# Optimization experiments

Hardware: AMD Instinct MI355X
Metric: run time of the kernel (lower is better)

## Reference

```python
import jax, jax.numpy as jnp
import numpy as np

WH = 7; WW = 7; N = WH * WW          # window tokens
C = 256; H = 8; D = C // H            # dim, heads, head_dim
SCALE = D ** -0.5
B = 4096                              # batch * num_windows
EPS = 1e-12


def _relative_position_index():
    coords = np.stack(np.meshgrid(np.arange(WH), np.arange(WW), indexing='ij'))  # [2,WH,WW]
    cf = coords.reshape(2, -1)                                                   # [2,N]
    rc = (cf[:, :, None] - cf[:, None, :]).transpose(1, 2, 0).astype(np.int64)   # [N,N,2]
    rc[..., 0] += WH - 1
    rc[..., 1] += WW - 1
    rc[..., 0] *= 2 * WW - 1
    return jnp.asarray(rc.sum(-1), jnp.int32)                                    # [N,N]


def _l2n_heads(x):
    # F.normalize default dim=1: normalize over the HEADS axis of [B,H,N,D]
    n = jnp.sqrt(jnp.sum(x * x, axis=1, keepdims=True))
    return x / jnp.maximum(n, EPS)


def setup_inputs() -> dict:
    key = jax.random.key(0)
    ks = jax.random.split(key, 12)
    p = lambda k, s: (0.02 * jax.random.normal(k, s, dtype=jnp.float32))
    return {
        'x1': jax.random.normal(ks[0], (B, N, C), dtype=jnp.float32),
        'x2': jax.random.normal(ks[1], (B, N, C), dtype=jnp.float32),
        'rel_index': _relative_position_index(),
        'kv1_w': p(ks[2], (2 * C, C)), 'kv1_b': jnp.zeros((2 * C,), jnp.float32),
        'kv2_w': p(ks[3], (2 * C, C)), 'kv2_b': jnp.zeros((2 * C,), jnp.float32),
        'q_w': p(ks[4], (C, C)), 'q_b': jnp.zeros((C,), jnp.float32),
        'rpb_table': p(ks[5], ((2 * WH - 1) * (2 * WW - 1), H)),
        'proj1_w': p(ks[6], (C, C)), 'proj1_b': jnp.zeros((C,), jnp.float32),
        'proj2_w': p(ks[7], (C, C)), 'proj2_b': jnp.zeros((C,), jnp.float32),
    }


def reference(x1, x2, rel_index, kv1_w, kv1_b, kv2_w, kv2_b, q_w, q_b,
              rpb_table, proj1_w, proj1_b, proj1=None, proj2=None, **_unused):
    del proj1, proj2
    raise NotImplementedError


def _forward(x1, x2, rel_index, kv1_w, kv1_b, kv2_w, kv2_b, q_w, q_b,
             rpb_table, proj1_w, proj1_b, proj2_w, proj2_b):
    def split_kv(x, w, b):
        kv = (x @ w.T + b).reshape(B, N, 2, H, D).transpose(2, 0, 3, 1, 4)  # [2,B,H,N,D]
        return kv[0], kv[1]

    k1, v1 = split_kv(x1, kv1_w, kv1_b)
    k2, v2 = split_kv(x2, kv2_w, kv2_b)

    q = (jnp.abs(x2 - x1) @ q_w.T + q_b).reshape(B, N, H, D).transpose(0, 2, 1, 3)  # [B,H,N,D]
    q = q * SCALE

    bias = rpb_table[rel_index.reshape(-1)].reshape(N, N, H).transpose(2, 0, 1)  # [H,N,N]

    # branch 1: attend q -> k2/v2
    attn = jnp.einsum('bhnd,bhmd->bhnm', _l2n_heads(q), _l2n_heads(k2)) + bias[None]
    attn = jax.nn.softmax(attn, axis=-1)
    o1 = (jnp.einsum('bhnm,bhmd->bhnd', attn, v2) - q).transpose(0, 2, 1, 3).reshape(B, N, C)
    o1 = o1 @ proj1_w.T + proj1_b

    # branch 2: q rescaled again, attend -> k1/v1
    q = q * SCALE
    attn = jnp.einsum('bhnd,bhmd->bhnm', _l2n_heads(q), _l2n_heads(k1)) + bias[None]
    attn = jax.nn.softmax(attn, axis=-1)
    o2 = (jnp.einsum('bhnm,bhmd->bhnd', attn, v1) - q).transpose(0, 2, 1, 3).reshape(B, N, C)
    o2 = o2 @ proj2_w.T + proj2_b
    return o1, o2


def reference(x1, x2, rel_index, kv1_w, kv1_b, kv2_w, kv2_b, q_w, q_b,
              rpb_table, proj1_w, proj1_b, proj2_w, proj2_b):
    return _forward(x1, x2, rel_index, kv1_w, kv1_b, kv2_w, kv2_b, q_w, q_b,
                    rpb_table, proj1_w, proj1_b, proj2_w, proj2_b)
```

## Files before the change

kernel.cpp:

```cpp
#include <hip/hip_runtime.h>
#include <hip/hip_bf16.h>


typedef __attribute__((ext_vector_type(8))) short short8;
typedef __attribute__((ext_vector_type(4))) float f32x4;

#define NTOK 49
#define NWIN 4096
#define MROWS 200704
#define NMT 3136
#define SCALE 0.17677669529663687f

#define TQ_T   0
#define TKV1_T 16
#define TKV2_T 48
#define TP1_T  80
#define TP2_T  96

#define OFF_BIAS_B 917504ull
#define OFF_QN_B   1048576ull
#define OFF_NRM_B  103809024ull
#define OFF_KN2_B  129499136ull
#define OFF_KN1_B  232259584ull
#define OFF_V2_B   335020032ull
#define OFF_V1_B   437780480ull

__device__ __forceinline__ short f2b(float f) {
    union { float f; unsigned u; } v{f};
    unsigned r = v.u + 0x7fffu + ((v.u >> 16) & 1u);
    return (short)(r >> 16);
}
__device__ __forceinline__ float b2f(short s) {
    return __uint_as_float(((unsigned)(unsigned short)s) << 16);
}
__device__ __forceinline__ short8 pack8(float4 a, float4 b) {
    short8 s;
    s[0]=f2b(a.x); s[1]=f2b(a.y); s[2]=f2b(a.z); s[3]=f2b(a.w);
    s[4]=f2b(b.x); s[5]=f2b(b.y); s[6]=f2b(b.z); s[7]=f2b(b.w);
    return s;
}
__device__ __forceinline__ f32x4 mfma16(short8 a, short8 b, f32x4 c) {
    return __builtin_amdgcn_mfma_f32_16x16x32_bf16(a, b, c, 0, 0, 0);
}
__device__ __forceinline__ short8 g16(const short* p) { return *(const short8*)p; }
__device__ __forceinline__ short8 ld16r128(const short* base, int row, int m8) {
    return *(const short8*)((const char*)base + row*128 + ((m8*2) ^ ((row&7)<<4)));
}
__device__ __forceinline__ void st2r128(short* base, int row, int m, short v) {
    *(short*)((char*)base + row*128 + ((m*2) ^ ((row&7)<<4))) = v;
}
__device__ __forceinline__ void gl16(const void* g, void* l) {
    __builtin_amdgcn_global_load_lds(
        (const __attribute__((address_space(1))) unsigned*)g,
        (__attribute__((address_space(3))) unsigned*)l, 16, 0, 0);
}
__device__ __forceinline__ short8 ldb(const short* tile, int lr, int lg, int kb) {
    return *(const short8*)((const char*)tile + lr*512
                            + ((kb*64 + lg*16) ^ ((lr&7)<<4)));
}

__global__ void prep_w(const float* __restrict__ qw, const float* __restrict__ kv1,
                       const float* __restrict__ kv2, const float* __restrict__ p1,
                       const float* __restrict__ p2, short* __restrict__ ws) {
    int i = blockIdx.x * 256 + threadIdx.x;
    int e = i * 8;
    const float* src; int rel, tbase;
    if      (e < 65536)  { src = qw;  rel = e;          tbase = TQ_T;  }
    else if (e < 196608) { src = kv1; rel = e - 65536;  tbase = TKV1_T; }
    else if (e < 327680) { src = kv2; rel = e - 196608; tbase = TKV2_T; }
    else if (e < 393216) { src = p1;  rel = e - 327680; tbase = TP1_T; }
    else                 { src = p2;  rel = e - 393216; tbase = TP2_T; }
    int row = rel >> 8, col = rel & 255;
    short8 v;
#pragma unroll
    for (int k = 0; k < 8; ++k) v[k] = f2b(src[rel + k]);
    char* dst = (char*)ws + (size_t)(tbase + (row >> 4)) * 8192
              + (row & 15) * 512 + ((col * 2) ^ ((row & 7) << 4));
    *(short8*)dst = v;
}

__global__ void k_bias(const int* __restrict__ rel_index,
                       const float* __restrict__ rpb, short* __restrict__ ws) {
    int i = blockIdx.x * 256 + threadIdx.x;
    int r  = i & 3;
    int nt = (i >> 2) & 3;
    int lr = (i >> 4) & 15;
    int lg = (i >> 8) & 3;
    int mt = (i >> 10) & 3;
    int h  = (i >> 12) & 7;
    int m  = 16*mt + 4*lg + r;
    int mc = 16*nt + lr;
    float v = 0.f;
    if (m < NTOK && mc < NTOK) v = rpb[rel_index[m*NTOK + mc]*8 + h];
    ((float*)((char*)ws + OFF_BIAS_B))[i] = v;
}

__global__ __launch_bounds__(256, 3)
void k_qkv(const float* __restrict__ x1, const float* __restrict__ x2,
           const float* __restrict__ kv1_b, const float* __restrict__ kv2_b,
           const float* __restrict__ q_b, short* __restrict__ ws)
{
    __shared__ short Bt[2][4096];

    const int t    = (int)threadIdx.x;
    const int wv   = t >> 6;
    const int lane = t & 63;
    const int lr   = t & 15;
    const int lg   = (t >> 4) & 3;
    const int bid  = (int)blockIdx.x;
    const int type = bid % 3;
    const int mt   = bid / 3;
    const int ar   = mt*64 + 16*wv + lr;

    unsigned widr[4], tokr[4];
#pragma unroll
    for (int r = 0; r < 4; ++r) {
        unsigned n = (unsigned)(mt*64 + 16*wv + 4*lg + r);
        widr[r] = n / 49u; tokr[r] = n - widr[r]*49u;
    }

    const char* tb = (const char*)ws
        + (size_t)(type == 0 ? TQ_T : (type == 1 ? TKV2_T : TKV1_T)) * 8192;

#define STAGE(J, B) do {                                                  \
        const char* g_ = tb + (size_t)(J)*8192 + wv*2048 + lane*16;       \
        char* l_ = (char*)Bt[(B)] + wv*2048 + lane*16;                    \
        gl16(g_, l_); gl16(g_ + 1024, l_ + 1024);                         \
    } while (0)

    if (type == 0) {
        short8 ad[8];
#pragma unroll
        for (int kb = 0; kb < 8; ++kb) {
            const float* pa = x2 + (size_t)ar*256 + kb*32 + lg*8;
            const float* pc = x1 + (size_t)ar*256 + kb*32 + lg*8;
            float4 a0 = *(const float4*)pa, a1 = *(const float4*)(pa+4);
            float4 c0 = *(const float4*)pc, c1 = *(const float4*)(pc+4);
            float4 d0 = make_float4(fabsf(a0.x-c0.x), fabsf(a0.y-c0.y),
                                    fabsf(a0.z-c0.z), fabsf(a0.w-c0.w));
            float4 d1 = make_float4(fabsf(a1.x-c1.x), fabsf(a1.y-c1.y),
                                    fabsf(a1.z-c1.z), fabsf(a1.w-c1.w));
            ad[kb] = pack8(d0, d1);
        }
        STAGE(0, 0);
        __syncthreads();
        f32x4 qa[16];
#pragma unroll
        for (int j = 0; j < 16; ++j) {
            if (j < 15) STAGE(j+1, (j+1)&1);
            const short* bt = Bt[j&1];
            f32x4 acc = {0.f,0.f,0.f,0.f};
#pragma unroll
            for (int kb = 0; kb < 8; ++kb) acc = mfma16(ad[kb], ldb(bt, lr, lg, kb), acc);
            float bj = q_b[j*16 + lr];
#pragma unroll
            for (int r = 0; r < 4; ++r) acc[r] = (acc[r] + bj) * SCALE;
            qa[j] = acc;
            __syncthreads();
        }
        short* qn  = (short*)((char*)ws + OFF_QN_B);
        float* nrm = (float*)((char*)ws + OFF_NRM_B);
#pragma unroll
        for (int r = 0; r < 4; ++r) {
            float s0 = 0.f, s1 = 0.f;
#pragma unroll
            for (int jj = 0; jj < 8; ++jj) {
                float v0 = qa[2*jj][r], v1 = qa[2*jj+1][r];
                s0 = fmaf(v0, v0, s0); s1 = fmaf(v1, v1, s1);
            }
            float n0 = fmaxf(sqrtf(s0), 1e-12f), n1 = fmaxf(sqrtf(s1), 1e-12f);
            unsigned n = widr[r]*49u + tokr[r];
            nrm[(size_t)n*32 + lr]      = n0;
            nrm[(size_t)n*32 + 16 + lr] = n1;
            float ri0 = 1.0f/n0, ri1 = 1.0f/n1;
            size_t base = ((size_t)widr[r]*392 + tokr[r])*32;
#pragma unroll
            for (int j = 0; j < 16; ++j) {
                int h = j >> 1, p = j & 1;
                qn[base + h*1568 + 16*p + lr] = f2b(qa[j][r] * (p ? ri1 : ri0));
            }
        }
    } else {
        const float* xp  = (type == 1) ? x2 : x1;
        const float* kvb = (type == 1) ? kv2_b : kv1_b;
        short* knp = (short*)((char*)ws + ((type == 1) ? OFF_KN2_B : OFF_KN1_B));
        short* vp  = (short*)((char*)ws + ((type == 1) ? OFF_V2_B  : OFF_V1_B));

        short8 ad[8];
#pragma unroll
        for (int kb = 0; kb < 8; ++kb) {
            const float* pa = xp + (size_t)ar*256 + kb*32 + lg*8;
            float4 a0 = *(const float4*)pa, a1 = *(const float4*)(pa+4);
            ad[kb] = pack8(a0, a1);
        }
        size_t base[4];
#pragma unroll
        for (int r = 0; r < 4; ++r) base[r] = ((size_t)widr[r]*392 + tokr[r])*32;

        STAGE(0, 0);
        __syncthreads();
        f32x4 ka[16];
#pragma unroll
        for (int j = 0; j < 32; ++j) {
            if (j < 31) STAGE(j+1, (j+1)&1);
            const short* bt = Bt[j&1];
            f32x4 acc = {0.f,0.f,0.f,0.f};
#pragma unroll
            for (int kb = 0; kb < 8; ++kb) acc = mfma16(ad[kb], ldb(bt, lr, lg, kb), acc);
            if (j < 16) {
                float bj = kvb[j*16 + lr];
#pragma unroll
                for (int r = 0; r < 4; ++r) acc[r] += bj;
                ka[j] = acc;
            } else {
                const int jv = j - 16;
                float bj = kvb[256 + jv*16 + lr];
                int h = jv >> 1, p = jv & 1;
#pragma unroll
                for (int r = 0; r < 4; ++r)
                    vp[base[r] + h*1568 + 16*p + lr] = f2b(acc[r] + bj);
            }
            __syncthreads();
        }
#pragma unroll
        for (int r = 0; r < 4; ++r) {
            float s0 = 0.f, s1 = 0.f;
#pragma unroll
            for (int jj = 0; jj < 8; ++jj) {
                float v0 = ka[2*jj][r], v1 = ka[2*jj+1][r];
                s0 = fmaf(v0, v0, s0); s1 = fmaf(v1, v1, s1);
            }
            float ri0 = 1.0f/fmaxf(sqrtf(s0), 1e-12f);
            float ri1 = 1.0f/fmaxf(sqrtf(s1), 1e-12f);
#pragma unroll
            for (int j = 0; j < 16; ++j) {
                int h = j >> 1, p = j & 1;
                knp[base[r] + h*1568 + 16*p + lr] = f2b(ka[j][r] * (p ? ri1 : ri0));
            }
        }
    }
#undef STAGE
}

__global__ __launch_bounds__(512, 2)
void k_attn(short* __restrict__ ws)
{
    __shared__ short OP[NTOK*256];
    __shared__ short PS[8*16*64];

    const int t  = (int)threadIdx.x;
    const int h  = t >> 6;
    const int lr = t & 15;
    const int lg = (t >> 4) & 3;
    const int bid = (int)blockIdx.x;
    const int wid = bid >> 1;
    const int br  = bid & 1;

    const short* qn  = (const short*)((const char*)ws + OFF_QN_B);
    const float* nrm = (const float*)((const char*)ws + OFF_NRM_B);
    const float* bias_t = (const float*)((const char*)ws + OFF_BIAS_B);
    short* Pb = PS + h*1024;
    const int khbase = (wid*8 + h)*49;

    const short* knp = (const short*)((const char*)ws + (br ? OFF_KN1_B : OFF_KN2_B));
    const short* vp  = (const short*)((const char*)ws + (br ? OFF_V1_B  : OFF_V2_B));
    short* opre = (short*)((char*)ws + (br ? OFF_KN1_B : OFF_KN2_B));
    const float subscale = br ? SCALE : 1.0f;

    short8 kf[4];
#pragma unroll
    for (int nt = 0; nt < 4; ++nt) {
        int n = min(16*nt + lr, NTOK-1);
        kf[nt] = g16(knp + (size_t)(khbase + n)*32 + lg*8);
    }
    short8 vf[2][2];
#pragma unroll
    for (int dt = 0; dt < 2; ++dt)
#pragma unroll
        for (int st = 0; st < 2; ++st) {
            short8 s8;
#pragma unroll
            for (int e = 0; e < 8; ++e) {
                int tok = st*32 + lg*8 + e;
                short v_ = 0;
                if (tok < NTOK) v_ = vp[(size_t)(khbase + tok)*32 + 16*dt + lr];
                s8[e] = v_;
            }
            vf[dt][st] = s8;
        }

#pragma unroll 1
    for (int mt = 0; mt < 4; ++mt) {
        int mrow = min(16*mt + lr, NTOK-1);
        short8 aq = g16(qn + (size_t)(khbase + mrow)*32 + lg*8);
        f32x4 S[4];
#pragma unroll
        for (int nt = 0; nt < 4; ++nt) {
            f32x4 z = {0.f,0.f,0.f,0.f};
            S[nt] = mfma16(aq, kf[nt], z);
        }
        const float4* bp4 = (const float4*)(bias_t + ((((h*4 + mt)*4 + lg)*16) + lr)*16);
        float4 bv[4];
#pragma unroll
        for (int nt = 0; nt < 4; ++nt) bv[nt] = bp4[nt];
        float sv[4][4];
#pragma unroll
        for (int nt = 0; nt < 4; ++nt) {
            bool ms = (16*nt + lr) >= NTOK;
            sv[nt][0] = ms ? -1e30f : (S[nt][0] + bv[nt].x);
            sv[nt][1] = ms ? -1e30f : (S[nt][1] + bv[nt].y);
            sv[nt][2] = ms ? -1e30f : (S[nt][2] + bv[nt].z);
            sv[nt][3] = ms ? -1e30f : (S[nt][3] + bv[nt].w);
        }
        float isum[4];
#pragma unroll
        for (int r = 0; r < 4; ++r) {
            float mx = fmaxf(fmaxf(sv[0][r], sv[1][r]), fmaxf(sv[2][r], sv[3][r]));
#pragma unroll
            for (int d = 1; d < 16; d <<= 1) mx = fmaxf(mx, __shfl_xor(mx, d));
            float e0 = __expf(sv[0][r]-mx), e1 = __expf(sv[1][r]-mx);
            float e2 = __expf(sv[2][r]-mx), e3 = __expf(sv[3][r]-mx);
            float sm = (e0+e1) + (e2+e3);
#pragma unroll
            for (int d = 1; d < 16; d <<= 1) sm += __shfl_xor(sm, d);
            isum[r] = 1.0f / sm;
            int pr = 4*lg + r;
            st2r128(Pb, pr,      lr, f2b(e0));
            st2r128(Pb, pr, 16 + lr, f2b(e1));
            st2r128(Pb, pr, 32 + lr, f2b(e2));
            st2r128(Pb, pr, 48 + lr, f2b(e3));
        }
        short8 pa0 = ld16r128(Pb, lr, lg*8);
        short8 pa1 = ld16r128(Pb, lr, 32 + lg*8);
#pragma unroll
        for (int dt = 0; dt < 2; ++dt) {
            f32x4 acc = {0.f,0.f,0.f,0.f};
            acc = mfma16(pa0, vf[dt][0], acc);
            acc = mfma16(pa1, vf[dt][1], acc);
#pragma unroll
            for (int r = 0; r < 4; ++r) {
                int m = 16*mt + 4*lg + r;
                int me = min(m, NTOK-1);
                int d = 16*dt + lr;
                float qv = b2f(qn[(size_t)(khbase + me)*32 + d]);
                float nv = nrm[((size_t)wid*NTOK + me)*32 + d];
                float o = acc[r]*isum[r] - qv*nv*subscale;
                if (m < NTOK) OP[m*256 + h*32 + d] = f2b(o);
            }
        }
    }
    __syncthreads();
    {
        const short8* sp = (const short8*)OP;
        short8* dp = (short8*)(opre + (size_t)wid*NTOK*256);
        for (int i = t; i < NTOK*256/8; i += 512) dp[i] = sp[i];
    }
}

__global__ __launch_bounds__(256, 3)
void k_proj(const float* __restrict__ p1_b, const float* __restrict__ p2_b,
            const short* __restrict__ ws, float* __restrict__ out)
{
    __shared__ short Bt[2][4096];

    const int t    = (int)threadIdx.x;
    const int wv   = t >> 6;
    const int lane = t & 63;
    const int lr   = t & 15;
    const int lg   = (t >> 4) & 3;
    const int bid  = (int)blockIdx.x;
    const int br   = bid & 1;
    const int mt   = bid >> 1;
    const int ar   = mt*64 + 16*wv + lr;

    const char* tb = (const char*)ws + (size_t)(br ? TP2_T : TP1_T) * 8192;
    const short* op  = (const short*)((const char*)ws + (br ? OFF_KN1_B : OFF_KN2_B));
    const float* pjb = br ? p2_b : p1_b;
    float* outp = out + (size_t)br*((size_t)MROWS*256);

    short8 ad[8];
#pragma unroll
    for (int kb = 0; kb < 8; ++kb) ad[kb] = g16(op + (size_t)ar*256 + kb*32 + lg*8);

#define STAGE(J, B) do {                                                  \
        const char* g_ = tb + (size_t)(J)*8192 + wv*2048 + lane*16;       \
        char* l_ = (char*)Bt[(B)] + wv*2048 + lane*16;                    \
        gl16(g_, l_); gl16(g_ + 1024, l_ + 1024);                         \
    } while (0)

    STAGE(0, 0);
    __syncthreads();
#pragma unroll 1
    for (int j = 0; j < 16; ++j) {
        if (j < 15) STAGE(j+1, (j+1)&1);
        const short* bt = Bt[j&1];
        f32x4 acc = {0.f,0.f,0.f,0.f};
#pragma unroll
        for (int kb = 0; kb < 8; ++kb) acc = mfma16(ad[kb], ldb(bt, lr, lg, kb), acc);
        float bj = pjb[j*16 + lr];
#pragma unroll
        for (int r = 0; r < 4; ++r) {
            int n = mt*64 + 16*wv + 4*lg + r;
            outp[(size_t)n*256 + j*16 + lr] = acc[r] + bj;
        }
        __syncthreads();
    }
#undef STAGE
}

extern "C" void kernel_launch(void* const* d_in, const int* in_sizes, int n_in,
                              void* d_out, int out_size, void* d_ws, size_t ws_size,
                              hipStream_t stream) {
    (void)in_sizes; (void)n_in; (void)ws_size; (void)out_size;
    const float* x1   = (const float*)d_in[0];
    const float* x2   = (const float*)d_in[1];
    const int*   rel  = (const int*)  d_in[2];
    const float* kv1w = (const float*)d_in[3];
    const float* kv1b = (const float*)d_in[4];
    const float* kv2w = (const float*)d_in[5];
    const float* kv2b = (const float*)d_in[6];
    const float* qw   = (const float*)d_in[7];
    const float* qb   = (const float*)d_in[8];
    const float* rpb  = (const float*)d_in[9];
    const float* p1w  = (const float*)d_in[10];
    const float* p1b  = (const float*)d_in[11];
    const float* p2w  = (const float*)d_in[12];
    const float* p2b  = (const float*)d_in[13];
    float* out = (float*)d_out;
    short* ws  = (short*)d_ws;

    hipLaunchKernelGGL(prep_w, dim3(224), dim3(256), 0, stream,
                       qw, kv1w, kv2w, p1w, p2w, ws);
    hipLaunchKernelGGL(k_bias, dim3(128), dim3(256), 0, stream,
                       rel, rpb, ws);
    hipLaunchKernelGGL(k_qkv, dim3(NMT*3), dim3(256), 0, stream,
                       x1, x2, kv1b, kv2b, qb, ws);
    hipLaunchKernelGGL(k_attn, dim3(NWIN*2), dim3(512), 0, stream, ws);
    hipLaunchKernelGGL(k_proj, dim3(NMT*2), dim3(256), 0, stream,
                       p1b, p2b, (const short*)ws, out);
}
```

Baseline: 856.7 us.

## Fuse output projection into attention kernel, dropping intermediate workspace round-trip

The attention kernel now keeps its per-window output in swizzled shared memory and runs the output projection directly from there. It stages projection weight tiles into LDS with double buffering and writes fp32 results plus bias straight to the output, so the separate projection kernel goes away. This removes the bf16 intermediate write and reread through global memory and one kernel launch. In exchange, shared memory per block grows by 32KB, and each window's 49 rows are padded to 64 in the MFMA tiles, wasting some compute. The extra LDS may also hurt occupancy.

```diff
diff --git a/kernel.cpp b/kernel.cpp
--- a/kernel.cpp
+++ b/kernel.cpp
@@ -43,6 +43,12 @@
     return __builtin_amdgcn_mfma_f32_16x16x32_bf16(a, b, c, 0, 0, 0);
 }
 __device__ __forceinline__ short8 g16(const short* p) { return *(const short8*)p; }
+__device__ __forceinline__ short8 ld16(const short* base, int row, int c8) {
+    return *(const short8*)((const char*)base + row*512 + ((c8*2) ^ ((row&7)<<4)));
+}
+__device__ __forceinline__ void st2(short* base, int row, int c, short v) {
+    *(short*)((char*)base + row*512 + ((c*2) ^ ((row&7)<<4))) = v;
+}
 __device__ __forceinline__ short8 ld16r128(const short* base, int row, int m8) {
     return *(const short8*)((const char*)base + row*128 + ((m8*2) ^ ((row&7)<<4)));
 }
@@ -243,10 +249,12 @@
 }
 
 __global__ __launch_bounds__(512, 2)
-void k_attn(short* __restrict__ ws)
+void k_attn(const float* __restrict__ p1_b, const float* __restrict__ p2_b,
+            short* __restrict__ ws, float* __restrict__ out)
 {
     __shared__ short OP[NTOK*256];
     __shared__ short PS[8*16*64];
+    __shared__ short Bt[2][8192];
 
     const int t  = (int)threadIdx.x;
     const int h  = t >> 6;
@@ -264,7 +272,6 @@
 
     const short* knp = (const short*)((const char*)ws + (br ? OFF_KN1_B : OFF_KN2_B));
     const short* vp  = (const short*)((const char*)ws + (br ? OFF_V1_B  : OFF_V2_B));
-    short* opre = (short*)((char*)ws + (br ? OFF_KN1_B : OFF_KN2_B));
     const float subscale = br ? SCALE : 1.0f;
 
     short8 kf[4];
@@ -345,67 +352,49 @@
                 float qv = b2f(qn[(size_t)(khbase + me)*32 + d]);
                 float nv = nrm[((size_t)wid*NTOK + me)*32 + d];
                 float o = acc[r]*isum[r] - qv*nv*subscale;
-                if (m < NTOK) OP[m*256 + h*32 + d] = f2b(o);
+                if (m < NTOK) st2(OP, m, h*32 + d, f2b(o));
             }
         }
     }
     __syncthreads();
+
     {
-        const short8* sp = (const short8*)OP;
-        short8* dp = (short8*)(opre + (size_t)wid*NTOK*256);
-        for (int i = t; i < NTOK*256/8; i += 512) dp[i] = sp[i];
+        const int pm = h & 3, pn = h >> 2;
+        const char* tb = (const char*)ws + (size_t)(br ? TP2_T : TP1_T) * 8192;
+        const float* pjb = br ? p2_b : p1_b;
+        float* outp = out + (size_t)br*((size_t)MROWS*256) + (size_t)wid*(NTOK*256);
+        const int parow = min(16*pm + lr, NTOK-1);
+
+        short8 ad[8];
+#pragma unroll
+        for (int kb = 0; kb < 8; ++kb) ad[kb] = ld16(OP, parow, kb*32 + lg*8);
+
+#define STAGEP(JJ, B) do {                                                \
+        const char* g_ = tb + (size_t)(JJ)*16384 + t*16;                  \
+        char* l_ = (char*)Bt[(B)] + t*16;                                 \
+        gl16(g_, l_); gl16(g_ + 8192, l_ + 8192);                         \
+    } while (0)
+
+        STAGEP(0, 0);
+        __syncthreads();
+#pragma unroll 1
+        for (int jj = 0; jj < 8; ++jj) {
+            if (jj < 7) STAGEP(jj+1, (jj+1)&1);
+            const short* bt = (const short*)((const char*)Bt[jj&1] + pn*8192);
+            f32x4 acc = {0.f,0.f,0.f,0.f};
+#pragma unroll
+            for (int kb = 0; kb < 8; ++kb) acc = mfma16(ad[kb], ldb(bt, lr, lg, kb), acc);
+            const int t16 = 2*jj + pn;
+            float bj = pjb[t16*16 + lr];
+#pragma unroll
+            for (int r = 0; r < 4; ++r) {
+                int n = 16*pm + 4*lg + r;
+                if (n < NTOK) outp[(size_t)n*256 + 16*t16 + lr] = acc[r] + bj;
+            }
+            __syncthreads();
+        }
+#undef STAGEP
     }
-}
-
-__global__ __launch_bounds__(256, 3)
-void k_proj(const float* __restrict__ p1_b, const float* __restrict__ p2_b,
-            const short* __restrict__ ws, float* __restrict__ out)
-{
-    __shared__ short Bt[2][4096];
-
-    const int t    = (int)threadIdx.x;
-    const int wv   = t >> 6;
-    const int lane = t & 63;
-    const int lr   = t & 15;
-    const int lg   = (t >> 4) & 3;
-    const int bid  = (int)blockIdx.x;
-    const int br   = bid & 1;
-    const int mt   = bid >> 1;
-    const int ar   = mt*64 + 16*wv + lr;
-
-    const char* tb = (const char*)ws + (size_t)(br ? TP2_T : TP1_T) * 8192;
-    const short* op  = (const short*)((const char*)ws + (br ? OFF_KN1_B : OFF_KN2_B));
-    const float* pjb = br ? p2_b : p1_b;
-    float* outp = out + (size_t)br*((size_t)MROWS*256);
-
-    short8 ad[8];
-#pragma unroll
-    for (int kb = 0; kb < 8; ++kb) ad[kb] = g16(op + (size_t)ar*256 + kb*32 + lg*8);
-
-#define STAGE(J, B) do {                                                  \
-        const char* g_ = tb + (size_t)(J)*8192 + wv*2048 + lane*16;       \
-        char* l_ = (char*)Bt[(B)] + wv*2048 + lane*16;                    \
-        gl16(g_, l_); gl16(g_ + 1024, l_ + 1024);                         \
-    } while (0)
-
-    STAGE(0, 0);
-    __syncthreads();
-#pragma unroll 1
-    for (int j = 0; j < 16; ++j) {
-        if (j < 15) STAGE(j+1, (j+1)&1);
-        const short* bt = Bt[j&1];
-        f32x4 acc = {0.f,0.f,0.f,0.f};
-#pragma unroll
-        for (int kb = 0; kb < 8; ++kb) acc = mfma16(ad[kb], ldb(bt, lr, lg, kb), acc);
-        float bj = pjb[j*16 + lr];
-#pragma unroll
-        for (int r = 0; r < 4; ++r) {
-            int n = mt*64 + 16*wv + 4*lg + r;
-            outp[(size_t)n*256 + j*16 + lr] = acc[r] + bj;
-        }
-        __syncthreads();
-    }
-#undef STAGE
 }
 
 extern "C" void kernel_launch(void* const* d_in, const int* in_sizes, int n_in,
@@ -435,7 +424,6 @@
                        rel, rpb, ws);
     hipLaunchKernelGGL(k_qkv, dim3(NMT*3), dim3(256), 0, stream,
                        x1, x2, kv1b, kv2b, qb, ws);
-    hipLaunchKernelGGL(k_attn, dim3(NWIN*2), dim3(512), 0, stream, ws);
-    hipLaunchKernelGGL(k_proj, dim3(NMT*2), dim3(256), 0, stream,
-                       p1b, p2b, (const short*)ws, out);
-}
+    hipLaunchKernelGGL(k_attn, dim3(NWIN*2), dim3(512), 0, stream,
+                       p1b, p2b, ws, out);
+}
```

New measurement: 891.7 us. 4.1% more time.
